# Kernel tuning notes

Measured on AMD Instinct MI355X. Metric: run time of the kernel, lower is better.

Reference implementation:

```python
import jax, jax.numpy as jnp
import numpy as np

B, T, D, H, L = 4, 128, 768, 770, 40  # batch, token_num, bert dim, head hidden, n_labels


def setup_inputs() -> dict:
    key = jax.random.key(0)
    ks = jax.random.split(key, 7)
    hidden = jax.random.normal(ks[0], (B, T + 1, D), dtype=jnp.float32)
    pred_spans = jnp.sort(jax.random.randint(ks[1], (B, 2), 0, T), axis=1)
    span_avail = jax.random.randint(ks[2], (T, T), 0, 2).astype(jnp.int32)
    # torch nn.Linear: weight init N(0, 0.02), bias init N(0, 1) (normal_(bias, 0) -> mean=0, std=1)
    W1 = (jax.random.normal(ks[3], (2 * D + 1, H)) * 0.02).astype(jnp.float32)
    b1 = jax.random.normal(ks[4], (H,), dtype=jnp.float32)
    W2 = (jax.random.normal(ks[5], (H, L)) * 0.02).astype(jnp.float32)
    b2 = jax.random.normal(ks[6], (L,), dtype=jnp.float32)
    return {"hidden": hidden, "W1": W1, "b1": b1, "W2": W2, "b2": b2,
            "pred_spans": pred_spans, "span_avail": span_avail, "token_num": T}


def reference(hidden, W1, b1, W2, b2, pred_spans, span_avail, token_num):
    # vecs[i] = hidden[:, i+1, :]  (skip [CLS])
    vecs = hidden[:, 1:token_num + 1, :]                      # [B, T, D]
    Bv, Tv, Dv = vecs.shape
    starts = pred_spans[:, 0][:, None, None]                  # [B,1,1]
    ends = pred_spans[:, 1][:, None, None]
    ii = jnp.arange(Tv)[:, None]                              # [T,1]
    jj = jnp.arange(Tv)[None, :]                              # [1,T]
    # indication: 2 if (i,j) == pred span; 1 if strictly inside span with i<=j; else 0
    is_full = (ii == starts) & (jj == ends)                   # [B,T,T]
    inside = (starts <= ii) & (ii <= jj) & (jj <= ends) & (~is_full)
    ind = (2 * is_full + inside).astype(hidden.dtype)         # [B,T,T]
    fi = jnp.broadcast_to(vecs[:, :, None, :], (Bv, Tv, Tv, Dv))
    fj = jnp.broadcast_to(vecs[:, None, :, :], (Bv, Tv, Tv, Dv))
    feat = jnp.concatenate([fi, fj, ind[..., None]], axis=-1)  # [B,T,T,2D+1]
    h = jax.nn.relu(feat @ W1 + b1)                            # [B,T,T,H]
    out = h @ W2 + b2                                          # [B,T,T,L]
    # unavailable spans contribute a zeros row (original appends `zeros`)
    mask = (span_avail >= 1)[None, :, :, None]
    out = jnp.where(mask, out, jnp.zeros((), out.dtype))
    out = out.reshape(Bv, Tv * Tv, -1)                         # span index c = i*T + j
    return jax.nn.log_softmax(out, axis=1)
```

## Files before the change

### kernel.cpp

```cpp
#include <hip/hip_runtime.h>
#include <math.h>

#define BB 4
#define TT 128
#define DD 768
#define HD 770
#define HP 800
#define LL 40
#define TP1 129

typedef __attribute__((ext_vector_type(8))) short s16x8;
typedef __attribute__((ext_vector_type(4))) float f32x4;

#define P_OFF   0
#define Q_OFF   409600
#define W2F_OFF 819200
#define BF1_OFF 838400
#define ACC_OFF 1440512

__device__ __forceinline__ unsigned pkbf(float a, float b) {
    unsigned ua = __float_as_uint(a);
    unsigned ub = __float_as_uint(b);
    return ((ua + 0x8000u) >> 16) | ((ub + 0x8000u) & 0xffff0000u);
}
__device__ __forceinline__ unsigned rne1(float v) {
    unsigned x = __float_as_uint(v);
    return (x + 0x7fffu + ((x >> 16) & 1u)) >> 16;
}

__global__ __launch_bounds__(256) void kPrep(const float* __restrict__ W1,
                                             const float* __restrict__ W2,
                                             float* __restrict__ Q,
                                             unsigned* __restrict__ W2f,
                                             unsigned* __restrict__ Bf1,
                                             float* __restrict__ accum) {
    const int bx = blockIdx.x;
    const int tid = threadIdx.x;
    if (bx < 19) {
        int u = bx * 256 + tid;
        if (u >= 4800) return;
        int nt = u / 1600;
        int rem = u - nt * 1600;
        int ks = rem >> 6;
        int lane = rem & 63;
        int kbase = ks * 32 + ((lane >> 4) << 3);
        int l = nt * 16 + (lane & 15);
        unsigned pk[4];
        #pragma unroll
        for (int sp = 0; sp < 4; ++sp) {
            unsigned w[2];
            #pragma unroll
            for (int e = 0; e < 2; ++e) {
                int k = kbase + 2 * sp + e;
                float v = (k < HD && l < LL) ? W2[k * LL + l] : 0.0f;
                w[e] = rne1(v);
            }
            pk[sp] = w[0] | (w[1] << 16);
        }
        ((uint4*)W2f)[u] = make_uint4(pk[0], pk[1], pk[2], pk[3]);
    } else if (bx < 607) {
        int u = (bx - 19) * 256 + tid;
        int lane = u & 63;
        int g = u >> 6;
        int ks = g % 24;
        int g2 = g / 24;
        int nt = g2 % 49;
        int half = g2 / 49;
        int kbase = ks * 32 + ((lane >> 4) << 3);
        int h = nt * 16 + (lane & 15);
        int row0 = half * DD + kbase;
        unsigned pk[4];
        #pragma unroll
        for (int sp = 0; sp < 4; ++sp) {
            unsigned w[2];
            #pragma unroll
            for (int e = 0; e < 2; ++e) {
                float v = (h < HD) ? W1[(size_t)(row0 + 2 * sp + e) * HD + h] : 0.0f;
                w[e] = rne1(v);
            }
            pk[sp] = w[0] | (w[1] << 16);
        }
        ((uint4*)Bf1)[u] = make_uint4(pk[0], pk[1], pk[2], pk[3]);
    } else {
        int u = (bx - 607) * 256 + tid;
        if (u < 160) accum[u] = 0.0f;
        int u2 = u - 160;
        if (u2 >= 0 && u2 < 512 * 30) {
            int row = u2 / 30;
            int h = HD + (u2 - row * 30);
            Q[(size_t)row * HP + h] = 0.0f;
        }
    }
}

__global__ __launch_bounds__(256) void kA(const float* __restrict__ hidden,
                                          const unsigned* __restrict__ Bf1,
                                          const float* __restrict__ b1,
                                          float* __restrict__ P,
                                          float* __restrict__ Q) {
    const int tid = threadIdx.x;
    const int w = blockIdx.x * 4 + (tid >> 6);
    const int lane = tid & 63;
    const int mband = w & 31;
    const int nt = w >> 5;
    const int b  = mband >> 3;
    const int tt = mband & 7;

    const float* __restrict__ Arow =
        hidden + (size_t)(b * TP1 + 1 + tt * 16 + (lane & 15)) * DD + ((lane >> 4) << 3);
    const uint4* __restrict__ B0 = (const uint4*)Bf1 + ((size_t)nt * 24) * 64 + lane;
    const uint4* __restrict__ B1 = (const uint4*)Bf1 + ((size_t)(49 + nt) * 24) * 64 + lane;

    f32x4 a0 = (f32x4){0.f,0.f,0.f,0.f};
    f32x4 a1 = (f32x4){0.f,0.f,0.f,0.f};

    #pragma unroll 4
    for (int ks = 0; ks < 24; ++ks) {
        float4 x0 = *(const float4*)(Arow + ks * 32);
        float4 x1 = *(const float4*)(Arow + ks * 32 + 4);
        union { unsigned u[4]; s16x8 v; } af;
        af.u[0] = pkbf(x0.x, x0.y); af.u[1] = pkbf(x0.z, x0.w);
        af.u[2] = pkbf(x1.x, x1.y); af.u[3] = pkbf(x1.z, x1.w);
        union { uint4 q; s16x8 v; } bf0, bf1;
        bf0.q = B0[ks * 64];
        bf1.q = B1[ks * 64];
        a0 = __builtin_amdgcn_mfma_f32_16x16x32_bf16(af.v, bf0.v, a0, 0, 0, 0);
        a1 = __builtin_amdgcn_mfma_f32_16x16x32_bf16(af.v, bf1.v, a1, 0, 0, 0);
    }

    const int col = lane & 15;
    const int h = nt * 16 + col;
    if (h < HD) {
        const float bv = b1[h];
        const int quad = lane >> 4;
        #pragma unroll
        for (int r = 0; r < 4; ++r) {
            int t = tt * 16 + quad * 4 + r;
            size_t row = (size_t)(b * TT + t) * HP;
            P[row + h] = a0[r] + bv;
            Q[row + h] = a1[r];
        }
    }
}

__global__ __launch_bounds__(256) void kB(const float* __restrict__ P,
                                          const float* __restrict__ Q,
                                          const float* __restrict__ W1,
                                          const unsigned* __restrict__ Bfrag,
                                          const float* __restrict__ b2,
                                          const int* __restrict__ spans,
                                          const int* __restrict__ avail,
                                          float* __restrict__ out,
                                          float* __restrict__ accum) {
    __shared__ unsigned Sb[2][128 * 20];
    __shared__ float var[3 * HP];
    __shared__ int avi[TT];
    __shared__ float sred[192];

    const int i = blockIdx.x;
    const int b = blockIdx.y;
    const int tid = threadIdx.x;
    const int wave = tid >> 6;
    const int lane = tid & 63;

    const int start = spans[b * 2];
    const int end   = spans[b * 2 + 1];

    const int jS = tid >> 1;
    const int hh = (tid & 1) << 4;
    int indS;
    {
        bool isfull = (i == start) && (jS == end);
        bool inside = (start <= i) && (i <= jS) && (jS <= end) && !isfull;
        indS = isfull ? 2 : (inside ? 1 : 0);
    }

    {
        const float* Pi  = P + (size_t)(b * TT + i) * HP;
        const float* w1L = W1 + (size_t)2 * DD * HD;
        for (int h = tid; h < HP; h += 256) {
            float pv = (h < HD) ? Pi[h] : 0.0f;
            float wv = (h < HD) ? w1L[h] : 0.0f;
            var[h]          = pv;
            var[HP + h]     = pv + wv;
            var[2*HP + h]   = pv + wv + wv;
        }
        if (tid < TT) avi[tid] = avail[i * TT + tid];
    }
    __syncthreads();

    const float* Qj = Q + (size_t)(b * TT + jS) * HP;
    const float* vb = var + indS * HP;

    auto form = [&](int c, int p) {
        const int h0 = c * 32 + hh;
        const float4* qp = (const float4*)(Qj + h0);
        float4 q0 = qp[0], q1 = qp[1], q2 = qp[2], q3 = qp[3];
        const float4* vp = (const float4*)(vb + h0);
        float4 v0 = vp[0], v1 = vp[1], v2 = vp[2], v3 = vp[3];
        float s0 = fmaxf(v0.x + q0.x, 0.f), s1 = fmaxf(v0.y + q0.y, 0.f);
        float s2 = fmaxf(v0.z + q0.z, 0.f), s3 = fmaxf(v0.w + q0.w, 0.f);
        float s4 = fmaxf(v1.x + q1.x, 0.f), s5 = fmaxf(v1.y + q1.y, 0.f);
        float s6 = fmaxf(v1.z + q1.z, 0.f), s7 = fmaxf(v1.w + q1.w, 0.f);
        float s8 = fmaxf(v2.x + q2.x, 0.f), s9 = fmaxf(v2.y + q2.y, 0.f);
        float sa = fmaxf(v2.z + q2.z, 0.f), sb_ = fmaxf(v2.w + q2.w, 0.f);
        float sc = fmaxf(v3.x + q3.x, 0.f), sd = fmaxf(v3.y + q3.y, 0.f);
        float se = fmaxf(v3.z + q3.z, 0.f), sf = fmaxf(v3.w + q3.w, 0.f);
        uint4* dst = (uint4*)(&Sb[p][jS * 20 + (hh >> 1)]);
        dst[0] = make_uint4(pkbf(s0,s1), pkbf(s2,s3), pkbf(s4,s5), pkbf(s6,s7));
        dst[1] = make_uint4(pkbf(s8,s9), pkbf(sa,sb_), pkbf(sc,sd), pkbf(se,sf));
    };

    f32x4 acc[2][3];
    #pragma unroll
    for (int mt = 0; mt < 2; ++mt)
        #pragma unroll
        for (int nt = 0; nt < 3; ++nt)
            acc[mt][nt] = (f32x4){0.f, 0.f, 0.f, 0.f};

    form(0, 0);
    __syncthreads();

    const int arow0 = (wave * 32 + (lane & 15)) * 20 + ((lane >> 4) << 2);
    for (int c = 0; c < 25; ++c) {
        const int p = c & 1;
        s16x8 bf0 = *(const s16x8*)(Bfrag + (( 0 + c) * 64 + lane) * 4);
        s16x8 bf1 = *(const s16x8*)(Bfrag + ((25 + c) * 64 + lane) * 4);
        s16x8 bf2 = *(const s16x8*)(Bfrag + ((50 + c) * 64 + lane) * 4);
        s16x8 af0 = *(const s16x8*)(&Sb[p][arow0]);
        s16x8 af1 = *(const s16x8*)(&Sb[p][arow0 + 16 * 20]);
        if (c + 1 < 25) form(c + 1, p ^ 1);
        acc[0][0] = __builtin_amdgcn_mfma_f32_16x16x32_bf16(af0, bf0, acc[0][0], 0, 0, 0);
        acc[0][1] = __builtin_amdgcn_mfma_f32_16x16x32_bf16(af0, bf1, acc[0][1], 0, 0, 0);
        acc[0][2] = __builtin_amdgcn_mfma_f32_16x16x32_bf16(af0, bf2, acc[0][2], 0, 0, 0);
        acc[1][0] = __builtin_amdgcn_mfma_f32_16x16x32_bf16(af1, bf0, acc[1][0], 0, 0, 0);
        acc[1][1] = __builtin_amdgcn_mfma_f32_16x16x32_bf16(af1, bf1, acc[1][1], 0, 0, 0);
        acc[1][2] = __builtin_amdgcn_mfma_f32_16x16x32_bf16(af1, bf2, acc[1][2], 0, 0, 0);
        __syncthreads();
    }

    float bias[3];
    #pragma unroll
    for (int nt = 0; nt < 3; ++nt) {
        int l = nt * 16 + (lane & 15);
        bias[nt] = (l < LL) ? b2[l] : 0.0f;
    }
    const int jr0 = wave * 32 + ((lane >> 4) << 2);
    float sE[3] = {0.f, 0.f, 0.f};
    #pragma unroll
    for (int mt = 0; mt < 2; ++mt) {
        #pragma unroll
        for (int r = 0; r < 4; ++r) {
            int j = jr0 + mt * 16 + r;
            bool msk = avi[j] >= 1;
            size_t rowoff = ((size_t)(b * (TT * TT) + i * TT + j)) * LL;
            #pragma unroll
            for (int nt = 0; nt < 3; ++nt) {
                int l = nt * 16 + (lane & 15);
                if (l < LL) {
                    float val = msk ? (acc[mt][nt][r] + bias[nt]) : 0.0f;
                    out[rowoff + l] = val;
                    sE[nt] += __expf(val);
                }
            }
        }
    }
    #pragma unroll
    for (int nt = 0; nt < 3; ++nt) {
        float v = sE[nt];
        v += __shfl_xor(v, 16);
        v += __shfl_xor(v, 32);
        if (lane < 16) sred[wave * 48 + nt * 16 + lane] = v;
    }
    __syncthreads();
    if (tid < 48) {
        float t4 = sred[tid] + sred[48 + tid] + sred[96 + tid] + sred[144 + tid];
        if (tid < LL) atomicAdd(&accum[b * LL + tid], t4);
    }
}

__global__ __launch_bounds__(256) void kD(float* __restrict__ out,
                                          const float* __restrict__ accum) {
    const int idx = blockIdx.x * 256 + threadIdx.x;
    const int e = idx * 4;
    const int b = e / (TT * TT * LL);
    const int l = e % LL;
    float4 v = ((float4*)out)[idx];
    const float* ac = accum + b * LL + l;
    v.x -= __logf(ac[0]); v.y -= __logf(ac[1]);
    v.z -= __logf(ac[2]); v.w -= __logf(ac[3]);
    ((float4*)out)[idx] = v;
}

extern "C" void kernel_launch(void* const* d_in, const int* in_sizes, int n_in,
                              void* d_out, int out_size, void* d_ws, size_t ws_size,
                              hipStream_t stream) {
    const float* hidden = (const float*)d_in[0];
    const float* W1     = (const float*)d_in[1];
    const float* b1     = (const float*)d_in[2];
    const float* W2     = (const float*)d_in[3];
    const float* b2     = (const float*)d_in[4];
    const int*   spans  = (const int*)d_in[5];
    const int*   avail  = (const int*)d_in[6];
    float* out = (float*)d_out;
    float* ws  = (float*)d_ws;

    float*    P     = ws + P_OFF;
    float*    Q     = ws + Q_OFF;
    unsigned* W2f   = (unsigned*)(ws + W2F_OFF);
    unsigned* Bf1   = (unsigned*)(ws + BF1_OFF);
    float*    accum = ws + ACC_OFF;

    kPrep<<<dim3(668),     dim3(256), 0, stream>>>(W1, W2, Q, W2f, Bf1, accum);
    kA   <<<dim3(392),     dim3(256), 0, stream>>>(hidden, Bf1, b1, P, Q);
    kB   <<<dim3(TT, BB),  dim3(256), 0, stream>>>(P, Q, W1, W2f, b2, spans, avail, out, accum);
    kD   <<<dim3(2560),    dim3(256), 0, stream>>>(out, accum);
}
```

Before: 128.6 us.

## Build MFMA A-fragments directly in registers, dropping LDS staging and barriers

In kB, each lane now builds its bf16 A-operand fragment for the hidden activations directly in registers from Q and the shared var table, instead of writing a double-buffered LDS tile that the other waves read back. This removes the shared staging buffer and the per-chunk __syncthreads across 25 iterations, letting waves proceed independently. The var table stride is padded from 800 to 808 floats, presumably to reduce LDS bank conflicts on the gathered reads. In exchange, Q reads are now strided per lane (8 floats per row across 16 rows) rather than cooperatively vectorised, which may raise global/L2 traffic.

Measured after the change: 141.8 us. +10.3%, slower.

```diff
diff --git a/kernel.cpp b/kernel.cpp
--- a/kernel.cpp
+++ b/kernel.cpp
@@ -8,6 +8,7 @@
 #define HP 800
 #define LL 40
 #define TP1 129
+#define VS 808
 
 typedef __attribute__((ext_vector_type(8))) short s16x8;
 typedef __attribute__((ext_vector_type(4))) float f32x4;
@@ -111,8 +112,8 @@
     const uint4* __restrict__ B0 = (const uint4*)Bf1 + ((size_t)nt * 24) * 64 + lane;
     const uint4* __restrict__ B1 = (const uint4*)Bf1 + ((size_t)(49 + nt) * 24) * 64 + lane;
 
-    f32x4 a0 = (f32x4){0.f,0.f,0.f,0.f};
-    f32x4 a1 = (f32x4){0.f,0.f,0.f,0.f};
+    f32x4 a0 = (f32x4){0.f, 0.f, 0.f, 0.f};
+    f32x4 a1 = (f32x4){0.f, 0.f, 0.f, 0.f};
 
     #pragma unroll 4
     for (int ks = 0; ks < 24; ++ks) {
@@ -146,14 +147,13 @@
 __global__ __launch_bounds__(256) void kB(const float* __restrict__ P,
                                           const float* __restrict__ Q,
                                           const float* __restrict__ W1,
-                                          const unsigned* __restrict__ Bfrag,
+                                          const unsigned* __restrict__ W2f,
                                           const float* __restrict__ b2,
                                           const int* __restrict__ spans,
                                           const int* __restrict__ avail,
                                           float* __restrict__ out,
                                           float* __restrict__ accum) {
-    __shared__ unsigned Sb[2][128 * 20];
-    __shared__ float var[3 * HP];
+    __shared__ float var[3 * VS];
     __shared__ int avi[TT];
     __shared__ float sred[192];
 
@@ -162,18 +162,11 @@
     const int tid = threadIdx.x;
     const int wave = tid >> 6;
     const int lane = tid & 63;
+    const int col  = lane & 15;
+    const int quad = lane >> 4;
 
     const int start = spans[b * 2];
     const int end   = spans[b * 2 + 1];
-
-    const int jS = tid >> 1;
-    const int hh = (tid & 1) << 4;
-    int indS;
-    {
-        bool isfull = (i == start) && (jS == end);
-        bool inside = (start <= i) && (i <= jS) && (jS <= end) && !isfull;
-        indS = isfull ? 2 : (inside ? 1 : 0);
-    }
 
     {
         const float* Pi  = P + (size_t)(b * TT + i) * HP;
@@ -182,34 +175,26 @@
             float pv = (h < HD) ? Pi[h] : 0.0f;
             float wv = (h < HD) ? w1L[h] : 0.0f;
             var[h]          = pv;
-            var[HP + h]     = pv + wv;
-            var[2*HP + h]   = pv + wv + wv;
+            var[VS + h]     = pv + wv;
+            var[2 * VS + h] = pv + wv + wv;
         }
         if (tid < TT) avi[tid] = avail[i * TT + tid];
     }
     __syncthreads();
 
-    const float* Qj = Q + (size_t)(b * TT + jS) * HP;
-    const float* vb = var + indS * HP;
-
-    auto form = [&](int c, int p) {
-        const int h0 = c * 32 + hh;
-        const float4* qp = (const float4*)(Qj + h0);
-        float4 q0 = qp[0], q1 = qp[1], q2 = qp[2], q3 = qp[3];
-        const float4* vp = (const float4*)(vb + h0);
-        float4 v0 = vp[0], v1 = vp[1], v2 = vp[2], v3 = vp[3];
-        float s0 = fmaxf(v0.x + q0.x, 0.f), s1 = fmaxf(v0.y + q0.y, 0.f);
-        float s2 = fmaxf(v0.z + q0.z, 0.f), s3 = fmaxf(v0.w + q0.w, 0.f);
-        float s4 = fmaxf(v1.x + q1.x, 0.f), s5 = fmaxf(v1.y + q1.y, 0.f);
-        float s6 = fmaxf(v1.z + q1.z, 0.f), s7 = fmaxf(v1.w + q1.w, 0.f);
-        float s8 = fmaxf(v2.x + q2.x, 0.f), s9 = fmaxf(v2.y + q2.y, 0.f);
-        float sa = fmaxf(v2.z + q2.z, 0.f), sb_ = fmaxf(v2.w + q2.w, 0.f);
-        float sc = fmaxf(v3.x + q3.x, 0.f), sd = fmaxf(v3.y + q3.y, 0.f);
-        float se = fmaxf(v3.z + q3.z, 0.f), sf = fmaxf(v3.w + q3.w, 0.f);
-        uint4* dst = (uint4*)(&Sb[p][jS * 20 + (hh >> 1)]);
-        dst[0] = make_uint4(pkbf(s0,s1), pkbf(s2,s3), pkbf(s4,s5), pkbf(s6,s7));
-        dst[1] = make_uint4(pkbf(s8,s9), pkbf(sa,sb_), pkbf(sc,sd), pkbf(se,sf));
-    };
+    int ind0, ind1, j0, j1;
+    {
+        j0 = (wave * 2 + 0) * 16 + col;
+        j1 = (wave * 2 + 1) * 16 + col;
+        bool f0 = (i == start) && (j0 == end);
+        bool f1 = (i == start) && (j1 == end);
+        ind0 = f0 ? 2 : (((start <= i) && (i <= j0) && (j0 <= end)) ? 1 : 0);
+        ind1 = f1 ? 2 : (((start <= i) && (i <= j1) && (j1 <= end)) ? 1 : 0);
+    }
+    const float* __restrict__ Q0 = Q + (size_t)(b * TT + j0) * HP;
+    const float* __restrict__ Q1 = Q + (size_t)(b * TT + j1) * HP;
+    const float* v0 = var + ind0 * VS;
+    const float* v1 = var + ind1 * VS;
 
     f32x4 acc[2][3];
     #pragma unroll
@@ -218,34 +203,53 @@
         for (int nt = 0; nt < 3; ++nt)
             acc[mt][nt] = (f32x4){0.f, 0.f, 0.f, 0.f};
 
-    form(0, 0);
-    __syncthreads();
-
-    const int arow0 = (wave * 32 + (lane & 15)) * 20 + ((lane >> 4) << 2);
-    for (int c = 0; c < 25; ++c) {
-        const int p = c & 1;
-        s16x8 bf0 = *(const s16x8*)(Bfrag + (( 0 + c) * 64 + lane) * 4);
-        s16x8 bf1 = *(const s16x8*)(Bfrag + ((25 + c) * 64 + lane) * 4);
-        s16x8 bf2 = *(const s16x8*)(Bfrag + ((50 + c) * 64 + lane) * 4);
-        s16x8 af0 = *(const s16x8*)(&Sb[p][arow0]);
-        s16x8 af1 = *(const s16x8*)(&Sb[p][arow0 + 16 * 20]);
-        if (c + 1 < 25) form(c + 1, p ^ 1);
-        acc[0][0] = __builtin_amdgcn_mfma_f32_16x16x32_bf16(af0, bf0, acc[0][0], 0, 0, 0);
-        acc[0][1] = __builtin_amdgcn_mfma_f32_16x16x32_bf16(af0, bf1, acc[0][1], 0, 0, 0);
-        acc[0][2] = __builtin_amdgcn_mfma_f32_16x16x32_bf16(af0, bf2, acc[0][2], 0, 0, 0);
-        acc[1][0] = __builtin_amdgcn_mfma_f32_16x16x32_bf16(af1, bf0, acc[1][0], 0, 0, 0);
-        acc[1][1] = __builtin_amdgcn_mfma_f32_16x16x32_bf16(af1, bf1, acc[1][1], 0, 0, 0);
-        acc[1][2] = __builtin_amdgcn_mfma_f32_16x16x32_bf16(af1, bf2, acc[1][2], 0, 0, 0);
-        __syncthreads();
+    #pragma unroll 5
+    for (int ks = 0; ks < 25; ++ks) {
+        const int h0 = ks * 32 + quad * 8;
+        union { uint4 q; s16x8 v; } bf0, bf1, bf2;
+        bf0.q = ((const uint4*)W2f)[( 0 + ks) * 64 + lane];
+        bf1.q = ((const uint4*)W2f)[(25 + ks) * 64 + lane];
+        bf2.q = ((const uint4*)W2f)[(50 + ks) * 64 + lane];
+        union { unsigned u[4]; s16x8 v; } a0, a1;
+        {
+            float4 qa = *(const float4*)(Q0 + h0);
+            float4 qb = *(const float4*)(Q0 + h0 + 4);
+            float4 va = *(const float4*)(v0 + h0);
+            float4 vb = *(const float4*)(v0 + h0 + 4);
+            float s0 = fmaxf(va.x + qa.x, 0.f), s1 = fmaxf(va.y + qa.y, 0.f);
+            float s2 = fmaxf(va.z + qa.z, 0.f), s3 = fmaxf(va.w + qa.w, 0.f);
+            float s4 = fmaxf(vb.x + qb.x, 0.f), s5 = fmaxf(vb.y + qb.y, 0.f);
+            float s6 = fmaxf(vb.z + qb.z, 0.f), s7 = fmaxf(vb.w + qb.w, 0.f);
+            a0.u[0] = pkbf(s0, s1); a0.u[1] = pkbf(s2, s3);
+            a0.u[2] = pkbf(s4, s5); a0.u[3] = pkbf(s6, s7);
+        }
+        {
+            float4 qa = *(const float4*)(Q1 + h0);
+            float4 qb = *(const float4*)(Q1 + h0 + 4);
+            float4 va = *(const float4*)(v1 + h0);
+            float4 vb = *(const float4*)(v1 + h0 + 4);
+            float s0 = fmaxf(va.x + qa.x, 0.f), s1 = fmaxf(va.y + qa.y, 0.f);
+            float s2 = fmaxf(va.z + qa.z, 0.f), s3 = fmaxf(va.w + qa.w, 0.f);
+            float s4 = fmaxf(vb.x + qb.x, 0.f), s5 = fmaxf(vb.y + qb.y, 0.f);
+            float s6 = fmaxf(vb.z + qb.z, 0.f), s7 = fmaxf(vb.w + qb.w, 0.f);
+            a1.u[0] = pkbf(s0, s1); a1.u[1] = pkbf(s2, s3);
+            a1.u[2] = pkbf(s4, s5); a1.u[3] = pkbf(s6, s7);
+        }
+        acc[0][0] = __builtin_amdgcn_mfma_f32_16x16x32_bf16(a0.v, bf0.v, acc[0][0], 0, 0, 0);
+        acc[0][1] = __builtin_amdgcn_mfma_f32_16x16x32_bf16(a0.v, bf1.v, acc[0][1], 0, 0, 0);
+        acc[0][2] = __builtin_amdgcn_mfma_f32_16x16x32_bf16(a0.v, bf2.v, acc[0][2], 0, 0, 0);
+        acc[1][0] = __builtin_amdgcn_mfma_f32_16x16x32_bf16(a1.v, bf0.v, acc[1][0], 0, 0, 0);
+        acc[1][1] = __builtin_amdgcn_mfma_f32_16x16x32_bf16(a1.v, bf1.v, acc[1][1], 0, 0, 0);
+        acc[1][2] = __builtin_amdgcn_mfma_f32_16x16x32_bf16(a1.v, bf2.v, acc[1][2], 0, 0, 0);
     }
 
     float bias[3];
     #pragma unroll
     for (int nt = 0; nt < 3; ++nt) {
-        int l = nt * 16 + (lane & 15);
+        int l = nt * 16 + col;
         bias[nt] = (l < LL) ? b2[l] : 0.0f;
     }
-    const int jr0 = wave * 32 + ((lane >> 4) << 2);
+    const int jr0 = wave * 32 + (quad << 2);
     float sE[3] = {0.f, 0.f, 0.f};
     #pragma unroll
     for (int mt = 0; mt < 2; ++mt) {
@@ -256,7 +260,7 @@
             size_t rowoff = ((size_t)(b * (TT * TT) + i * TT + j)) * LL;
             #pragma unroll
             for (int nt = 0; nt < 3; ++nt) {
-                int l = nt * 16 + (lane & 15);
+                int l = nt * 16 + col;
                 if (l < LL) {
                     float val = msk ? (acc[mt][nt][r] + bias[nt]) : 0.0f;
                     out[rowoff + l] = val;
@@ -311,8 +315,8 @@
     unsigned* Bf1   = (unsigned*)(ws + BF1_OFF);
     float*    accum = ws + ACC_OFF;
 
-    kPrep<<<dim3(668),     dim3(256), 0, stream>>>(W1, W2, Q, W2f, Bf1, accum);
-    kA   <<<dim3(392),     dim3(256), 0, stream>>>(hidden, Bf1, b1, P, Q);
-    kB   <<<dim3(TT, BB),  dim3(256), 0, stream>>>(P, Q, W1, W2f, b2, spans, avail, out, accum);
-    kD   <<<dim3(2560),    dim3(256), 0, stream>>>(out, accum);
-}
+    kPrep<<<dim3(668),    dim3(256), 0, stream>>>(W1, W2, Q, W2f, Bf1, accum);
+    kA   <<<dim3(392),    dim3(256), 0, stream>>>(hidden, Bf1, b1, P, Q);
+    kB   <<<dim3(TT, BB), dim3(256), 0, stream>>>(P, Q, W1, W2f, b2, spans, avail, out, accum);
+    kD   <<<dim3(2560),   dim3(256), 0, stream>>>(out, accum);
+}
```
